# Kernel optimization log

Measured on AMD Instinct MI355X. Metric: run time of the kernel, lower is better.

## Reference

```python
import jax, jax.numpy as jnp
import numpy as np

WS = (3, 8, 8)          # (t, h, w) window
SHIFT = (0, 4, 4)
HEADS = 6
DIM = 120
HD = DIM // HEADS
SCALE = HD ** -0.5
N = WS[0] * WS[1] * WS[2]   # 192 tokens per window
NQ = N // 3                 # 64 query tokens (last frame)


def _rel_pos_index():
    cd, ch, cw = np.arange(WS[0]), np.arange(WS[1]), np.arange(WS[2])
    c2 = np.stack(np.meshgrid(cd, ch, cw, indexing='ij')).reshape(3, -1)      # (3, N)
    c1 = np.stack(np.meshgrid(np.arange(1), ch, cw, indexing='ij')).reshape(3, -1)  # (3, NQ)
    rel = (c1[:, :, None] - c2[:, None, :]).transpose(1, 2, 0)                # (NQ, N, 3)
    rel = rel + np.array([WS[0] - 1, WS[1] - 1, WS[2] - 1])
    idx = rel[..., 0] * (2 * WS[1] - 1) * (2 * WS[2] - 1) + rel[..., 1] * (2 * WS[2] - 1) + rel[..., 2]
    return idx.astype(np.int32)  # values in [0, 3*15*15)


def _shift_attn_mask(h, w):
    # standard Swin shifted-window mask, tiled over the 3 frames
    img = np.zeros((h, w), np.int32)
    cnt = 0
    for hs in (slice(0, -WS[1]), slice(-WS[1], -SHIFT[1]), slice(-SHIFT[1], None)):
        for ws_ in (slice(0, -WS[2]), slice(-WS[2], -SHIFT[2]), slice(-SHIFT[2], None)):
            img[hs, ws_] = cnt
            cnt += 1
    win = img.reshape(h // WS[1], WS[1], w // WS[2], WS[2]).transpose(0, 2, 1, 3).reshape(-1, WS[1] * WS[2])
    m2 = win[:, None, :] - win[:, :, None]
    m2 = np.where(m2 != 0, -100.0, 0.0).astype(np.float32)  # (nW, 64, 64)
    return np.tile(m2, (1, 3, 3))                            # (nW, 192, 192)


def setup_inputs() -> dict:
    key = jax.random.key(0)
    ks = jax.random.split(key, 10)
    b, t, h, w, c = 1, 3, 256, 256, DIM
    nW = (h // WS[1]) * (w // WS[2])
    B_ = b * nW
    return {
        'x': jax.random.normal(ks[0], (b, t, h, w, c), jnp.float32),
        'quary0': jax.random.normal(ks[1], (B_, NQ, c), jnp.float32),
        'quary1': jax.random.normal(ks[2], (B_, NQ, c), jnp.float32),
        'qkv_w': jax.random.normal(ks[3], (3 * c, c), jnp.float32) * 0.02,
        'qkv_b': jnp.zeros((3 * c,), jnp.float32),
        'proj_w': jax.random.normal(ks[4], (c, c), jnp.float32) * 0.02,
        'proj_b': jnp.zeros((c,), jnp.float32),
        'rpb_table': jax.random.normal(ks[5], (WS[0] * (2 * WS[1] - 1) * (2 * WS[2] - 1), HEADS), jnp.float32) * 0.02,
        'pm_w': jax.random.normal(ks[6], (1, c), jnp.float32) * 0.02,
        'pm_b': jnp.zeros((1,), jnp.float32),
        'attn_mask': jnp.asarray(_shift_attn_mask(h, w)),
        'rel_idx': jnp.asarray(_rel_pos_index()),
    }


def reference(x, quary0, quary1, qkv_w, qkv_b, proj_w, proj_b, rpb_table, pm_w, pm_b, attn_mask, rel_idx):
    b, t, h, w, c = x.shape
    # cyclic shift
    x = jnp.roll(x, (-SHIFT[0], -SHIFT[1], -SHIFT[2]), axis=(1, 2, 3))
    # window partition -> (B_, N, c)
    xw = x.reshape(b, t // WS[0], WS[0], h // WS[1], WS[1], w // WS[2], WS[2], c)
    xw = xw.transpose(0, 1, 3, 5, 2, 4, 6, 7).reshape(-1, N, c)
    B_ = xw.shape[0]
    # adaptive mask prediction (eval path: hard threshold; sigmoid(s/T)>=0.5 <=> s>=0)
    pred_q = jax.lax.stop_gradient(xw[:, 2 * NQ:, :])
    soft = jnp.abs(pred_q - quary0) @ pm_w.T + pm_b          # (B_, NQ, 1)
    pred = (soft >= 0).astype(x.dtype)
    # qkv
    qkv = (xw @ qkv_w.T + qkv_b).reshape(B_, N, 3, HEADS, HD).transpose(2, 0, 3, 1, 4)
    q = qkv[0][:, :, 2 * NQ:, :] * SCALE                      # (B_, H, NQ, hd)
    k, v = qkv[1], qkv[2]                                     # (B_, H, N, hd)
    attn = jnp.einsum('bhqd,bhkd->bhqk', q, k)                # (B_, H, NQ, N)
    # gathered relative position bias
    rpb = rpb_table[rel_idx.reshape(-1)].reshape(NQ, N, HEADS).transpose(2, 0, 1)
    attn = attn + rpb[None]
    # shift mask
    nW = attn_mask.shape[0]
    attn = attn.reshape(b, nW, HEADS, NQ, N) + attn_mask[None, :, None, 2 * NQ:, :]
    attn = jax.nn.softmax(attn.reshape(B_, HEADS, NQ, N), axis=-1)
    out = jnp.einsum('bhqk,bhkd->bqhd', attn, v).reshape(B_, NQ, c)
    # output projection + token-pruning blend (math-equivalent to gather/fill eval path)
    x1 = out @ proj_w.T + proj_b
    x_pred = x1 * pred + quary1 * (1.0 - pred)
    xo = jnp.concatenate([x_pred, pred], axis=-1)             # (B_, NQ, c+1)
    # single-frame window reverse
    xo = xo.reshape(b, h // WS[1], w // WS[2], WS[1], WS[2], c + 1)
    xo = xo.transpose(0, 1, 3, 2, 4, 5).reshape(b, h, w, c + 1)
    xo = jnp.roll(xo, (SHIFT[1], SHIFT[2]), axis=(1, 2))
    return xo
```

## Files before the change

### kernel.cpp

```cpp
#include <hip/hip_runtime.h>
#include <math.h>

#define NT 512

typedef __attribute__((ext_vector_type(8))) short s16x8;
typedef __attribute__((ext_vector_type(4))) float f32x4;

#define KVF_OFF 0
#define QF_OFF  73728
#define PJF_OFF 122880
#define RPB_OFF 172032

__device__ __forceinline__ unsigned short f2bf(float f) {
    union { float f; unsigned int i; } v; v.f = f;
    unsigned int x = v.i;
    x += 0x7fffu + ((x >> 16) & 1u);
    return (unsigned short)(x >> 16);
}

#define MFMA(a, b, c) __builtin_amdgcn_mfma_f32_16x16x32_bf16(a, b, c, 0, 0, 0)

__global__ void prep(const float* __restrict__ qkv_w,
                     const float* __restrict__ proj_w,
                     const float* __restrict__ rpb_table,
                     const int*   __restrict__ rel_idx,
                     unsigned char* __restrict__ wsb)
{
    int gid = blockIdx.x * blockDim.x + threadIdx.x;
    int nthr = gridDim.x * blockDim.x;
    unsigned short* KVF = (unsigned short*)(wsb + KVF_OFF);
    unsigned short* QF  = (unsigned short*)(wsb + QF_OFF);
    unsigned short* PJF = (unsigned short*)(wsb + PJF_OFF);
    float*          RPB = (float*)(wsb + RPB_OFF);

    for (int f = gid; f < 6 * 3 * 4 * 512; f += nthr) {
        int q = f & 511, rest = f >> 9;
        int kk = rest & 3, rest2 = rest >> 2;
        int nt = rest2 % 3, h = rest2 / 3;
        int ln = q >> 3, j = q & 7;
        int l15 = ln & 15, qd = ln >> 4;
        int nglob = nt * 16 + l15, k = kk * 32 + qd * 8 + j;
        float v = 0.f;
        if (k < 120 && nglob < 40) {
            int row = (nglob < 20) ? (120 + h * 20 + nglob) : (240 + h * 20 + nglob - 20);
            v = qkv_w[row * 120 + k];
        }
        KVF[f] = f2bf(v);
    }
    for (int f = gid; f < 6 * 2 * 4 * 512; f += nthr) {
        int q = f & 511, rest = f >> 9;
        int kk = rest & 3, rest2 = rest >> 2;
        int nt = rest2 & 1, h = rest2 >> 1;
        int ln = q >> 3, j = q & 7;
        int l15 = ln & 15, qd = ln >> 4;
        int nn = nt * 16 + l15, k = kk * 32 + qd * 8 + j;
        int row = h * 20 + nn;
        float v = (k < 120) ? qkv_w[row * 120 + k] : 0.f;
        QF[f] = f2bf(v);
    }
    for (int f = gid; f < 6 * 8 * 512; f += nthr) {
        int q = f & 511, rest = f >> 9;
        int nt = rest & 7, h = rest >> 3;
        int ln = q >> 3, j = q & 7;
        int l15 = ln & 15, qd = ln >> 4;
        int c = nt * 16 + l15, k = qd * 8 + j;
        float v = (k < 20 && c < 120) ? proj_w[c * 120 + h * 20 + k] : 0.f;
        PJF[f] = f2bf(v);
    }
    for (int i = gid; i < 6 * 64 * 192; i += nthr) {
        int n = i % 192, r = (i / 192) % 64, h = i / (192 * 64);
        RPB[i] = rpb_table[rel_idx[r * 192 + n] * 6 + h];
    }
}

__global__ __launch_bounds__(NT, 2)
void swin_mfma(const float* __restrict__ x,
               const float* __restrict__ quary0,
               const float* __restrict__ quary1,
               const float* __restrict__ qkv_b,
               const float* __restrict__ proj_b,
               const float* __restrict__ pm_w,
               const float* __restrict__ pm_b,
               const unsigned char* __restrict__ wsb,
               float* __restrict__ out)
{
    alignas(16) __shared__ unsigned short xw[192 * 120 + 8];
    alignas(16) __shared__ unsigned short ks[192 * 40];
    alignas(16) __shared__ unsigned short vt[2 * 32 * 200];
    alignas(16) __shared__ unsigned short ps[2 * 64 * 200];
    alignas(16) __shared__ unsigned short qs[64 * 40];
    alignas(16) __shared__ unsigned short oh[64 * 40];
    __shared__ float pred_s[64];
    __shared__ int grp_s[64];

    const int tid = threadIdx.x;
    const int wv = tid >> 6, ln = tid & 63;
    const int l15 = ln & 15, qd = ln >> 4;
    const int widx = blockIdx.x;
    const int wh = widx >> 5, ww = widx & 31;
    const float SCALE = 0.22360679774997896f;

    const unsigned short* KVF = (const unsigned short*)(wsb + KVF_OFF);
    const unsigned short* QF  = (const unsigned short*)(wsb + QF_OFF);
    const unsigned short* PJF = (const unsigned short*)(wsb + PJF_OFF);
    const float*          RPB = (const float*)(wsb + RPB_OFF);

    for (int e = tid; e < 192 * 30; e += NT) {
        int n = e / 30, c4 = e % 30;
        int f = n >> 6, ii = (n >> 3) & 7, jj = n & 7;
        int y0 = (wh * 8 + ii + 4) & 255;
        int x0 = (ww * 8 + jj + 4) & 255;
        float4 val = *(const float4*)(x + (((size_t)(f * 256 + y0)) * 256 + x0) * 120 + c4 * 4);
        unsigned int lo = (unsigned)f2bf(val.x) | ((unsigned)f2bf(val.y) << 16);
        unsigned int hi = (unsigned)f2bf(val.z) | ((unsigned)f2bf(val.w) << 16);
        unsigned int off = (unsigned)(n * 120 + c4 * 4);
        *(unsigned int*)(xw + off)     = lo;
        *(unsigned int*)(xw + off + 2) = hi;
    }
    if (tid < 8) xw[192 * 120 + tid] = 0;
    for (int e = tid; e < 192 * 12; e += NT) ks[(e / 12) * 40 + 20 + (e % 12)] = 0;
    for (int e = tid; e < 64 * 12;  e += NT) qs[(e / 12) * 40 + 20 + (e % 12)] = 0;
    for (int e = tid; e < 64 * 40;  e += NT) oh[e] = 0;
    for (int e = tid; e < 2 * 12 * 200; e += NT) {
        int b = e / 2400, rr = (e % 2400) / 200, cc = e % 200;
        vt[b * 6400 + (20 + rr) * 200 + cc] = 0;
    }
    if (tid < 64) {
        int ii = tid >> 3, jj = tid & 7;
        int y0 = (wh * 8 + ii + 4) & 255;
        int x0 = (ww * 8 + jj + 4) & 255;
        int hg = (y0 >= 248) + (y0 >= 252);
        int wg = (x0 >= 248) + (x0 >= 252);
        grp_s[tid] = hg * 3 + wg;
    }
    if (tid < 256) {
        int r = tid >> 2, j = tid & 3;
        int ii = r >> 3, jj = r & 7;
        int y0 = (wh * 8 + ii + 4) & 255;
        int x0 = (ww * 8 + jj + 4) & 255;
        const float* xr  = x + (((size_t)(2 * 256 + y0)) * 256 + x0) * 120;
        const float* q0r = quary0 + ((size_t)widx * 64 + r) * 120;
        float acc = 0.f;
        for (int ch = j * 30; ch < j * 30 + 30; ++ch)
            acc += fabsf(xr[ch] - q0r[ch]) * pm_w[ch];
        acc += __shfl_xor(acc, 1);
        acc += __shfl_xor(acc, 2);
        if (j == 0) pred_s[r] = (acc + pm_b[0] >= 0.f) ? 1.f : 0.f;
    }

    f32x4 pacc[8];
    #pragma unroll
    for (int i = 0; i < 8; ++i) { f32x4 z = {0.f,0.f,0.f,0.f}; pacc[i] = z; }

    __syncthreads();

    for (int h = 0; h < 7; ++h) {
        if (h < 6) {
            unsigned short* vtw = vt + (h & 1) * 6400;
            for (int e = wv; e < 44; e += 8) {
                if (e < 36) {
                    int mt = e % 12, nt = e / 12;
                    const unsigned short* arow  = xw + (mt * 16 + l15) * 120;
                    const unsigned short* bbase = KVF + ((h * 3 + nt) * 4) * 512 + ln * 8;
                    f32x4 acc = {0.f, 0.f, 0.f, 0.f};
                    #pragma unroll
                    for (int kk = 0; kk < 4; ++kk) {
                        s16x8 aF = *(const s16x8*)(arow + kk * 32 + qd * 8);
                        s16x8 bF = *(const s16x8*)(bbase + kk * 512);
                        acc = MFMA(aF, bF, acc);
                    }
                    int nglob = nt * 16 + l15;
                    if (nglob < 40) {
                        float bias = qkv_b[nglob < 20 ? (120 + h * 20 + nglob)
                                                      : (240 + h * 20 + nglob - 20)];
                        #pragma unroll
                        for (int reg = 0; reg < 4; ++reg) {
                            int tok = mt * 16 + qd * 4 + reg;
                            unsigned short vb = f2bf(acc[reg] + bias);
                            if (nglob < 20) ks[tok * 40 + nglob] = vb;
                            else            vtw[(nglob - 20) * 200 + tok] = vb;
                        }
                    }
                } else {
                    int t = e - 36, mt = t & 3, nt = t >> 2;
                    const unsigned short* arow  = xw + (128 + mt * 16 + l15) * 120;
                    const unsigned short* bbase = QF + ((h * 2 + nt) * 4) * 512 + ln * 8;
                    f32x4 acc = {0.f, 0.f, 0.f, 0.f};
                    #pragma unroll
                    for (int kk = 0; kk < 4; ++kk) {
                        s16x8 aF = *(const s16x8*)(arow + kk * 32 + qd * 8);
                        s16x8 bF = *(const s16x8*)(bbase + kk * 512);
                        acc = MFMA(aF, bF, acc);
                    }
                    int nn = nt * 16 + l15;
                    if (nn < 20) {
                        float bias = qkv_b[h * 20 + nn];
                        #pragma unroll
                        for (int reg = 0; reg < 4; ++reg)
                            qs[(mt * 16 + qd * 4 + reg) * 40 + nn] = f2bf((acc[reg] + bias) * SCALE);
                    }
                }
            }
        }
        __syncthreads();

        if (wv < 4) {
            if (h < 6) {
                const int mt = wv;
                s16x8 aF = *(const s16x8*)(qs + (mt * 16 + l15) * 40 + qd * 8);
                f32x4 sc[12];
                #pragma unroll
                for (int t = 0; t < 12; ++t) {
                    s16x8 bF = *(const s16x8*)(ks + (t * 16 + l15) * 40 + qd * 8);
                    f32x4 z = {0.f, 0.f, 0.f, 0.f};
                    sc[t] = MFMA(aF, bF, z);
                }
                int gk[12];
                #pragma unroll
                for (int t = 0; t < 12; ++t) gk[t] = grp_s[(t * 16 + l15) & 63];
                unsigned short* psw = ps + (h & 1) * 12800;
                #pragma unroll
                for (int reg = 0; reg < 4; ++reg) {
                    int r = mt * 16 + qd * 4 + reg;
                    int gq = grp_s[r];
                    const float* rrow = RPB + (size_t)(h * 64 + r) * 192;
                    float vals[12];
                    float m = -1e30f;
                    #pragma unroll
                    for (int t = 0; t < 12; ++t) {
                        float v = sc[t][reg] + rrow[t * 16 + l15]
                                + ((gq == gk[t]) ? 0.f : -100.f);
                        vals[t] = v; m = fmaxf(m, v);
                    }
                    m = fmaxf(m, __shfl_xor(m, 1));
                    m = fmaxf(m, __shfl_xor(m, 2));
                    m = fmaxf(m, __shfl_xor(m, 4));
                    m = fmaxf(m, __shfl_xor(m, 8));
                    float s = 0.f;
                    #pragma unroll
                    for (int t = 0; t < 12; ++t) {
                        float ev = __expf(vals[t] - m);
                        vals[t] = ev; s += ev;
                    }
                    s += __shfl_xor(s, 1);
                    s += __shfl_xor(s, 2);
                    s += __shfl_xor(s, 4);
                    s += __shfl_xor(s, 8);
                    float inv = 1.0f / s;
                    #pragma unroll
                    for (int t = 0; t < 12; ++t)
                        psw[r * 200 + t * 16 + l15] = f2bf(vals[t] * inv);
                }
            }
        } else if (h > 0) {
            const int hp = h - 1, mtc = wv - 4;
            const unsigned short* psb = ps + (hp & 1) * 12800;
            const unsigned short* vtb = vt + (hp & 1) * 6400;
            #pragma unroll
            for (int ntp = 0; ntp < 2; ++ntp) {
                f32x4 acc = {0.f, 0.f, 0.f, 0.f};
                const unsigned short* prow = psb + (mtc * 16 + l15) * 200;
                const unsigned short* vrow = vtb + (ntp * 16 + l15) * 200;
                #pragma unroll
                for (int kk = 0; kk < 6; ++kk) {
                    s16x8 aF = *(const s16x8*)(prow + kk * 32 + qd * 8);
                    s16x8 bF = *(const s16x8*)(vrow + kk * 32 + qd * 8);
                    acc = MFMA(aF, bF, acc);
                }
                int d = ntp * 16 + l15;
                if (d < 20) {
                    #pragma unroll
                    for (int reg = 0; reg < 4; ++reg)
                        oh[(mtc * 16 + qd * 4 + reg) * 40 + d] = f2bf(acc[reg]);
                }
            }
            s16x8 aP = *(const s16x8*)(oh + (mtc * 16 + l15) * 40 + qd * 8);
            #pragma unroll
            for (int nt = 0; nt < 8; ++nt) {
                s16x8 bF = *(const s16x8*)(PJF + (hp * 8 + nt) * 512 + ln * 8);
                pacc[nt] = MFMA(aP, bF, pacc[nt]);
            }
        }
        __syncthreads();
    }

    if (wv >= 4) {
        const int mtc = wv - 4;
        #pragma unroll
        for (int nt = 0; nt < 8; ++nt) {
            int c = nt * 16 + l15;
            if (c < 120) {
                float pb = proj_b[c];
                #pragma unroll
                for (int reg = 0; reg < 4; ++reg) {
                    int r = mtc * 16 + qd * 4 + reg;
                    float p = pred_s[r];
                    int ii = r >> 3, jj = r & 7;
                    int y0 = (wh * 8 + ii + 4) & 255;
                    int x0 = (ww * 8 + jj + 4) & 255;
                    float fin = (p != 0.f) ? (pacc[nt][reg] + pb)
                                           : quary1[(size_t)widx * 7680 + (size_t)r * 120 + c];
                    out[((size_t)(y0 * 256 + x0)) * 121 + c] = fin;
                }
            }
        }
    }
    if (tid < 64) {
        int r = tid;
        int ii = r >> 3, jj = r & 7;
        int y0 = (wh * 8 + ii + 4) & 255;
        int x0 = (ww * 8 + jj + 4) & 255;
        out[((size_t)(y0 * 256 + x0)) * 121 + 120] = pred_s[r];
    }
}

extern "C" void kernel_launch(void* const* d_in, const int* in_sizes, int n_in,
                              void* d_out, int out_size, void* d_ws, size_t ws_size,
                              hipStream_t stream) {
    const float* x        = (const float*)d_in[0];
    const float* quary0   = (const float*)d_in[1];
    const float* quary1   = (const float*)d_in[2];
    const float* qkv_w    = (const float*)d_in[3];
    const float* qkv_b    = (const float*)d_in[4];
    const float* proj_w   = (const float*)d_in[5];
    const float* proj_b   = (const float*)d_in[6];
    const float* rpb      = (const float*)d_in[7];
    const float* pm_w     = (const float*)d_in[8];
    const float* pm_b     = (const float*)d_in[9];
    const int*   rel_idx  = (const int*)d_in[11];
    float* out = (float*)d_out;
    unsigned char* wsb = (unsigned char*)d_ws;

    prep<<<128, 512, 0, stream>>>(qkv_w, proj_w, rpb, rel_idx, wsb);
    swin_mfma<<<1024, NT, 0, stream>>>(x, quary0, quary1, qkv_b, proj_b,
                                       pm_w, pm_b, wsb, out);
}
```

Before: 501.3 us.

## Halve block size and keep attention probabilities in registers via transposed MFMA

```diff
diff --git a/kernel.cpp b/kernel.cpp
--- a/kernel.cpp
+++ b/kernel.cpp
@@ -1,7 +1,7 @@
 #include <hip/hip_runtime.h>
 #include <math.h>
 
-#define NT 512
+#define NT 256
 
 typedef __attribute__((ext_vector_type(8))) short s16x8;
 typedef __attribute__((ext_vector_type(4))) float f32x4;
@@ -16,6 +16,9 @@
     unsigned int x = v.i;
     x += 0x7fffu + ((x >> 16) & 1u);
     return (unsigned short)(x >> 16);
+}
+__device__ __forceinline__ unsigned int pk2(float a, float b) {
+    return (unsigned int)f2bf(a) | ((unsigned int)f2bf(b) << 16);
 }
 
 #define MFMA(a, b, c) __builtin_amdgcn_mfma_f32_16x16x32_bf16(a, b, c, 0, 0, 0)
@@ -60,15 +63,15 @@
     }
     for (int f = gid; f < 6 * 8 * 512; f += nthr) {
         int q = f & 511, rest = f >> 9;
-        int nt = rest & 7, h = rest >> 3;
+        int ct = rest & 7, h = rest >> 3;
         int ln = q >> 3, j = q & 7;
         int l15 = ln & 15, qd = ln >> 4;
-        int c = nt * 16 + l15, k = qd * 8 + j;
+        int c = ct * 16 + l15, k = qd * 8 + j;
         float v = (k < 20 && c < 120) ? proj_w[c * 120 + h * 20 + k] : 0.f;
         PJF[f] = f2bf(v);
     }
-    for (int i = gid; i < 6 * 64 * 192; i += nthr) {
-        int n = i % 192, r = (i / 192) % 64, h = i / (192 * 64);
+    for (int i = gid; i < 6 * 192 * 64; i += nthr) {
+        int r = i & 63, n = (i >> 6) % 192, h = i / (192 * 64);
         RPB[i] = rpb_table[rel_idx[r * 192 + n] * 6 + h];
     }
 }
@@ -84,14 +87,13 @@
                const unsigned char* __restrict__ wsb,
                float* __restrict__ out)
 {
-    alignas(16) __shared__ unsigned short xw[192 * 120 + 8];
-    alignas(16) __shared__ unsigned short ks[192 * 40];
-    alignas(16) __shared__ unsigned short vt[2 * 32 * 200];
-    alignas(16) __shared__ unsigned short ps[2 * 64 * 200];
-    alignas(16) __shared__ unsigned short qs[64 * 40];
-    alignas(16) __shared__ unsigned short oh[64 * 40];
-    __shared__ float pred_s[64];
-    __shared__ int grp_s[64];
+    __shared__ alignas(16) unsigned char smem[79888];
+    unsigned short* xw = (unsigned short*)smem;
+    unsigned short* ks = (unsigned short*)(smem + 46096);
+    unsigned short* vt = (unsigned short*)(smem + 61456);
+    unsigned short* qs = (unsigned short*)(smem + 74256);
+    float* pred_s = (float*)(smem + 79376);
+    int*   grp_s  = (int*)(smem + 79632);
 
     const int tid = threadIdx.x;
     const int wv = tid >> 6, ln = tid & 63;
@@ -120,11 +122,7 @@
     if (tid < 8) xw[192 * 120 + tid] = 0;
     for (int e = tid; e < 192 * 12; e += NT) ks[(e / 12) * 40 + 20 + (e % 12)] = 0;
     for (int e = tid; e < 64 * 12;  e += NT) qs[(e / 12) * 40 + 20 + (e % 12)] = 0;
-    for (int e = tid; e < 64 * 40;  e += NT) oh[e] = 0;
-    for (int e = tid; e < 2 * 12 * 200; e += NT) {
-        int b = e / 2400, rr = (e % 2400) / 200, cc = e % 200;
-        vt[b * 6400 + (20 + rr) * 200 + cc] = 0;
-    }
+    for (int e = tid; e < 12 * 200; e += NT) vt[(20 + e / 200) * 200 + (e % 200)] = 0;
     if (tid < 64) {
         int ii = tid >> 3, jj = tid & 7;
         int y0 = (wh * 8 + ii + 4) & 255;
@@ -133,7 +131,7 @@
         int wg = (x0 >= 248) + (x0 >= 252);
         grp_s[tid] = hg * 3 + wg;
     }
-    if (tid < 256) {
+    {
         int r = tid >> 2, j = tid & 3;
         int ii = r >> 3, jj = r & 7;
         int y0 = (wh * 8 + ii + 4) & 255;
@@ -147,170 +145,181 @@
         acc += __shfl_xor(acc, 2);
         if (j == 0) pred_s[r] = (acc + pm_b[0] >= 0.f) ? 1.f : 0.f;
     }
+    __syncthreads();
+
+    const int q_l = wv * 16 + l15;
+    const int gq = grp_s[q_l];
+    unsigned long long mbits = 0ull;
+    #pragma unroll
+    for (int t = 0; t < 12; ++t)
+        #pragma unroll
+        for (int r = 0; r < 4; ++r) {
+            int tok = t * 16 + qd * 4 + r;
+            if (gq != grp_s[tok & 63]) mbits |= (1ull << (t * 4 + r));
+        }
+    const int srcA = (((qd * 2) & 3) << 4) | l15;
+    const int srcB = (((qd * 2 + 1) & 3) << 4) | l15;
+    const int msel = qd >> 1;
 
     f32x4 pacc[8];
     #pragma unroll
     for (int i = 0; i < 8; ++i) { f32x4 z = {0.f,0.f,0.f,0.f}; pacc[i] = z; }
 
-    __syncthreads();
-
-    for (int h = 0; h < 7; ++h) {
-        if (h < 6) {
-            unsigned short* vtw = vt + (h & 1) * 6400;
-            for (int e = wv; e < 44; e += 8) {
-                if (e < 36) {
-                    int mt = e % 12, nt = e / 12;
-                    const unsigned short* arow  = xw + (mt * 16 + l15) * 120;
-                    const unsigned short* bbase = KVF + ((h * 3 + nt) * 4) * 512 + ln * 8;
-                    f32x4 acc = {0.f, 0.f, 0.f, 0.f};
+    for (int h = 0; h < 6; ++h) {
+        for (int e = wv; e < 44; e += 4) {
+            if (e < 36) {
+                int mt = e % 12, nt = e / 12;
+                const unsigned short* arow  = xw + (mt * 16 + l15) * 120;
+                const unsigned short* bbase = KVF + ((h * 3 + nt) * 4) * 512 + ln * 8;
+                f32x4 acc = {0.f, 0.f, 0.f, 0.f};
+                #pragma unroll
+                for (int kk = 0; kk < 4; ++kk) {
+                    s16x8 aF = *(const s16x8*)(arow + kk * 32 + qd * 8);
+                    s16x8 bF = *(const s16x8*)(bbase + kk * 512);
+                    acc = MFMA(aF, bF, acc);
+                }
+                int nglob = nt * 16 + l15;
+                if (nglob < 40) {
+                    float bias = qkv_b[nglob < 20 ? (120 + h * 20 + nglob)
+                                                  : (240 + h * 20 + nglob - 20)];
                     #pragma unroll
-                    for (int kk = 0; kk < 4; ++kk) {
-                        s16x8 aF = *(const s16x8*)(arow + kk * 32 + qd * 8);
-                        s16x8 bF = *(const s16x8*)(bbase + kk * 512);
-                        acc = MFMA(aF, bF, acc);
-                    }
-                    int nglob = nt * 16 + l15;
-                    if (nglob < 40) {
-                        float bias = qkv_b[nglob < 20 ? (120 + h * 20 + nglob)
-                                                      : (240 + h * 20 + nglob - 20)];
-                        #pragma unroll
-                        for (int reg = 0; reg < 4; ++reg) {
-                            int tok = mt * 16 + qd * 4 + reg;
-                            unsigned short vb = f2bf(acc[reg] + bias);
-                            if (nglob < 20) ks[tok * 40 + nglob] = vb;
-                            else            vtw[(nglob - 20) * 200 + tok] = vb;
-                        }
-                    }
-                } else {
-                    int t = e - 36, mt = t & 3, nt = t >> 2;
-                    const unsigned short* arow  = xw + (128 + mt * 16 + l15) * 120;
-                    const unsigned short* bbase = QF + ((h * 2 + nt) * 4) * 512 + ln * 8;
-                    f32x4 acc = {0.f, 0.f, 0.f, 0.f};
-                    #pragma unroll
-                    for (int kk = 0; kk < 4; ++kk) {
-                        s16x8 aF = *(const s16x8*)(arow + kk * 32 + qd * 8);
-                        s16x8 bF = *(const s16x8*)(bbase + kk * 512);
-                        acc = MFMA(aF, bF, acc);
-                    }
-                    int nn = nt * 16 + l15;
-                    if (nn < 20) {
-                        float bias = qkv_b[h * 20 + nn];
-                        #pragma unroll
-                        for (int reg = 0; reg < 4; ++reg)
-                            qs[(mt * 16 + qd * 4 + reg) * 40 + nn] = f2bf((acc[reg] + bias) * SCALE);
+                    for (int reg = 0; reg < 4; ++reg) {
+                        int tok = mt * 16 + qd * 4 + reg;
+                        unsigned short vb = f2bf(acc[reg] + bias);
+                        if (nglob < 20) ks[tok * 40 + nglob] = vb;
+                        else            vt[(nglob - 20) * 200 + tok] = vb;
                     }
                 }
-            }
-        }
-        __syncthreads();
-
-        if (wv < 4) {
-            if (h < 6) {
-                const int mt = wv;
-                s16x8 aF = *(const s16x8*)(qs + (mt * 16 + l15) * 40 + qd * 8);
-                f32x4 sc[12];
+            } else {
+                int t = e - 36, mt = t & 3, nt = t >> 2;
+                const unsigned short* arow  = xw + (128 + mt * 16 + l15) * 120;
+                const unsigned short* bbase = QF + ((h * 2 + nt) * 4) * 512 + ln * 8;
+                f32x4 acc = {0.f, 0.f, 0.f, 0.f};
                 #pragma unroll
-                for (int t = 0; t < 12; ++t) {
-                    s16x8 bF = *(const s16x8*)(ks + (t * 16 + l15) * 40 + qd * 8);
-                    f32x4 z = {0.f, 0.f, 0.f, 0.f};
-                    sc[t] = MFMA(aF, bF, z);
+                for (int kk = 0; kk < 4; ++kk) {
+                    s16x8 aF = *(const s16x8*)(arow + kk * 32 + qd * 8);
+                    s16x8 bF = *(const s16x8*)(bbase + kk * 512);
+                    acc = MFMA(aF, bF, acc);
                 }
-                int gk[12];
-                #pragma unroll
-                for (int t = 0; t < 12; ++t) gk[t] = grp_s[(t * 16 + l15) & 63];
-                unsigned short* psw = ps + (h & 1) * 12800;
-                #pragma unroll
-                for (int reg = 0; reg < 4; ++reg) {
-                    int r = mt * 16 + qd * 4 + reg;
-                    int gq = grp_s[r];
-                    const float* rrow = RPB + (size_t)(h * 64 + r) * 192;
-                    float vals[12];
-                    float m = -1e30f;
+                int nn = nt * 16 + l15;
+                if (nn < 20) {
+                    float bias = qkv_b[h * 20 + nn];
                     #pragma unroll
-                    for (int t = 0; t < 12; ++t) {
-                        float v = sc[t][reg] + rrow[t * 16 + l15]
-                                + ((gq == gk[t]) ? 0.f : -100.f);
-                        vals[t] = v; m = fmaxf(m, v);
-                    }
-                    m = fmaxf(m, __shfl_xor(m, 1));
-                    m = fmaxf(m, __shfl_xor(m, 2));
-                    m = fmaxf(m, __shfl_xor(m, 4));
-                    m = fmaxf(m, __shfl_xor(m, 8));
-                    float s = 0.f;
-                    #pragma unroll
-                    for (int t = 0; t < 12; ++t) {
-                        float ev = __expf(vals[t] - m);
-                        vals[t] = ev; s += ev;
-                    }
-                    s += __shfl_xor(s, 1);
-                    s += __shfl_xor(s, 2);
-                    s += __shfl_xor(s, 4);
-                    s += __shfl_xor(s, 8);
-                    float inv = 1.0f / s;
-                    #pragma unroll
-                    for (int t = 0; t < 12; ++t)
-                        psw[r * 200 + t * 16 + l15] = f2bf(vals[t] * inv);
+                    for (int reg = 0; reg < 4; ++reg)
+                        qs[(mt * 16 + qd * 4 + reg) * 40 + nn] = f2bf((acc[reg] + bias) * SCALE);
                 }
             }
-        } else if (h > 0) {
-            const int hp = h - 1, mtc = wv - 4;
-            const unsigned short* psb = ps + (hp & 1) * 12800;
-            const unsigned short* vtb = vt + (hp & 1) * 6400;
+        }
+        __syncthreads();
+
+        const float* rbase = RPB + ((size_t)(h * 192 + qd * 4)) * 64 + q_l;
+        float vals[48];
+        #pragma unroll
+        for (int t = 0; t < 12; ++t)
             #pragma unroll
-            for (int ntp = 0; ntp < 2; ++ntp) {
-                f32x4 acc = {0.f, 0.f, 0.f, 0.f};
-                const unsigned short* prow = psb + (mtc * 16 + l15) * 200;
-                const unsigned short* vrow = vtb + (ntp * 16 + l15) * 200;
-                #pragma unroll
-                for (int kk = 0; kk < 6; ++kk) {
-                    s16x8 aF = *(const s16x8*)(prow + kk * 32 + qd * 8);
-                    s16x8 bF = *(const s16x8*)(vrow + kk * 32 + qd * 8);
-                    acc = MFMA(aF, bF, acc);
-                }
-                int d = ntp * 16 + l15;
-                if (d < 20) {
-                    #pragma unroll
-                    for (int reg = 0; reg < 4; ++reg)
-                        oh[(mtc * 16 + qd * 4 + reg) * 40 + d] = f2bf(acc[reg]);
-                }
+            for (int r = 0; r < 4; ++r)
+                vals[t * 4 + r] = rbase[(t * 16 + r) * 64]
+                                + (((mbits >> (t * 4 + r)) & 1ull) ? -100.f : 0.f);
+
+        const s16x8 bQ = *(const s16x8*)(qs + q_l * 40 + qd * 8);
+        f32x4 sc[12];
+        #pragma unroll
+        for (int t = 0; t < 12; ++t) {
+            s16x8 aK = *(const s16x8*)(ks + (t * 16 + l15) * 40 + qd * 8);
+            f32x4 z = {0.f, 0.f, 0.f, 0.f};
+            sc[t] = MFMA(aK, bQ, z);
+        }
+
+        float m = -1e30f;
+        #pragma unroll
+        for (int t = 0; t < 12; ++t)
+            #pragma unroll
+            for (int r = 0; r < 4; ++r) {
+                float v = vals[t * 4 + r] + sc[t][r];
+                vals[t * 4 + r] = v; m = fmaxf(m, v);
             }
-            s16x8 aP = *(const s16x8*)(oh + (mtc * 16 + l15) * 40 + qd * 8);
+        m = fmaxf(m, __shfl_xor(m, 16));
+        m = fmaxf(m, __shfl_xor(m, 32));
+        float s = 0.f;
+        #pragma unroll
+        for (int i = 0; i < 48; ++i) { float ev = __expf(vals[i] - m); vals[i] = ev; s += ev; }
+        s += __shfl_xor(s, 16);
+        s += __shfl_xor(s, 32);
+        float inv = 1.0f / s;
+
+        unsigned int plo[12], phi[12];
+        #pragma unroll
+        for (int t = 0; t < 12; ++t) {
+            plo[t] = pk2(vals[t * 4 + 0] * inv, vals[t * 4 + 1] * inv);
+            phi[t] = pk2(vals[t * 4 + 2] * inv, vals[t * 4 + 3] * inv);
+        }
+
+        f32x4 o0 = {0.f,0.f,0.f,0.f}, o1 = {0.f,0.f,0.f,0.f};
+        #pragma unroll
+        for (int kk = 0; kk < 6; ++kk) {
+            unsigned int a0 = __shfl(plo[2 * kk],     srcA);
+            unsigned int a1 = __shfl(plo[2 * kk + 1], srcA);
+            unsigned int b0 = __shfl(phi[2 * kk],     srcA);
+            unsigned int b1 = __shfl(phi[2 * kk + 1], srcA);
+            unsigned int c0 = __shfl(plo[2 * kk],     srcB);
+            unsigned int c1 = __shfl(plo[2 * kk + 1], srcB);
+            unsigned int d0 = __shfl(phi[2 * kk],     srcB);
+            unsigned int d1 = __shfl(phi[2 * kk + 1], srcB);
+            union { s16x8 v; unsigned int u[4]; } bf;
+            bf.u[0] = msel ? a1 : a0;
+            bf.u[1] = msel ? b1 : b0;
+            bf.u[2] = msel ? c1 : c0;
+            bf.u[3] = msel ? d1 : d0;
+            s16x8 aV0 = *(const s16x8*)(vt + l15 * 200 + kk * 32 + qd * 8);
+            s16x8 aV1 = *(const s16x8*)(vt + (16 + l15) * 200 + kk * 32 + qd * 8);
+            o0 = MFMA(aV0, bf.v, o0);
+            o1 = MFMA(aV1, bf.v, o1);
+        }
+
+        {
+            unsigned int ol0 = pk2(o0[0], o0[1]), oh0 = pk2(o0[2], o0[3]);
+            unsigned int ol1 = pk2(o1[0], o1[1]), oh1 = pk2(o1[2], o1[3]);
+            unsigned int w0a = __shfl(ol0, srcA), w0b = __shfl(ol1, srcA);
+            unsigned int w1a = __shfl(oh0, srcA), w1b = __shfl(oh1, srcA);
+            unsigned int w2a = __shfl(ol0, srcB), w2b = __shfl(ol1, srcB);
+            unsigned int w3a = __shfl(oh0, srcB), w3b = __shfl(oh1, srcB);
+            union { s16x8 v; unsigned int u[4]; } bo;
+            bo.u[0] = msel ? w0b : w0a;
+            bo.u[1] = msel ? w1b : w1a;
+            bo.u[2] = msel ? w2b : w2a;
+            bo.u[3] = msel ? w3b : w3a;
             #pragma unroll
-            for (int nt = 0; nt < 8; ++nt) {
-                s16x8 bF = *(const s16x8*)(PJF + (hp * 8 + nt) * 512 + ln * 8);
-                pacc[nt] = MFMA(aP, bF, pacc[nt]);
+            for (int ct = 0; ct < 8; ++ct) {
+                s16x8 aP = *(const s16x8*)(PJF + (h * 8 + ct) * 512 + ln * 8);
+                pacc[ct] = MFMA(aP, bo.v, pacc[ct]);
             }
         }
         __syncthreads();
     }
 
-    if (wv >= 4) {
-        const int mtc = wv - 4;
-        #pragma unroll
-        for (int nt = 0; nt < 8; ++nt) {
-            int c = nt * 16 + l15;
-            if (c < 120) {
-                float pb = proj_b[c];
-                #pragma unroll
-                for (int reg = 0; reg < 4; ++reg) {
-                    int r = mtc * 16 + qd * 4 + reg;
-                    float p = pred_s[r];
-                    int ii = r >> 3, jj = r & 7;
-                    int y0 = (wh * 8 + ii + 4) & 255;
-                    int x0 = (ww * 8 + jj + 4) & 255;
-                    float fin = (p != 0.f) ? (pacc[nt][reg] + pb)
-                                           : quary1[(size_t)widx * 7680 + (size_t)r * 120 + c];
-                    out[((size_t)(y0 * 256 + x0)) * 121 + c] = fin;
-                }
-            }
-        }
-    }
-    if (tid < 64) {
-        int r = tid;
+    float* xo = (float*)smem;
+    #pragma unroll
+    for (int ct = 0; ct < 8; ++ct)
+        #pragma unroll
+        for (int r = 0; r < 4; ++r) {
+            int c = ct * 16 + qd * 4 + r;
+            if (c < 120) xo[q_l * 129 + c] = pacc[ct][r];
+        }
+    __syncthreads();
+
+    for (int e = tid; e < 64 * 121; e += NT) {
+        int r = e / 121, c = e - r * 121;
         int ii = r >> 3, jj = r & 7;
         int y0 = (wh * 8 + ii + 4) & 255;
         int x0 = (ww * 8 + jj + 4) & 255;
-        out[((size_t)(y0 * 256 + x0)) * 121 + 120] = pred_s[r];
+        float p = pred_s[r];
+        float val;
+        if (c < 120)
+            val = (p != 0.f) ? (xo[r * 129 + c] + proj_b[c])
+                             : quary1[(size_t)widx * 7680 + (size_t)r * 120 + c];
+        else
+            val = p;
+        out[((size_t)(y0 * 256 + x0)) * 121 + c] = val;
     }
 }
 
```

Measured after the change: 457.8 us. -8.7%, faster.
